# Kernel optimization log

Measured on AMD Instinct MI355X. Metric: run time of the kernel, lower is better.

Reference implementation:

```python
import jax, jax.numpy as jnp
import numpy as np

B, N_FEAT, SEQ, E, H, V = 32, 196, 64, 1024, 1024, 32000


def setup_inputs() -> dict:
    key = jax.random.key(0)
    ks = jax.random.split(key, 16)
    s = 0.02
    return {
        "features": jax.random.normal(ks[0], (B, N_FEAT, E), jnp.float32),
        "captions": jax.random.randint(ks[1], (B, SEQ), 0, V),
        "max_seq_length": SEQ,
        # decoder embedding table (vocab, embed)
        "emb": jax.random.normal(ks[2], (V, E), jnp.float32) * s,
        # attention MLP: Linear(E->H), Tanh, Linear(H->1)
        "Wa1": jax.random.normal(ks[3], (H, E), jnp.float32) * s,
        "ba1": jnp.zeros((H,), jnp.float32),
        "Wa2": jax.random.normal(ks[4], (1, H), jnp.float32) * s,
        "ba2": jnp.zeros((1,), jnp.float32),
        # GRU (1 layer), input = concat(word_emb, context) -> E + H
        "W_ih": jax.random.normal(ks[5], (3 * H, E + H), jnp.float32) * s,
        "W_hh": jax.random.normal(ks[6], (3 * H, H), jnp.float32) * s,
        "b_ih": jnp.zeros((3 * H,), jnp.float32),
        "b_hh": jnp.zeros((3 * H,), jnp.float32),
        # output projection Linear(H -> V)
        "W_fc": jax.random.normal(ks[7], (V, H), jnp.float32) * s,
        "b_fc": jnp.zeros((V,), jnp.float32),
    }


def reference(features, captions, max_seq_length, emb, Wa1, ba1, Wa2, ba2,
              W_ih, W_hh, b_ih, b_hh, W_fc, b_fc):
    # words: (B, S, E)
    words = emb[captions]
    # combined: (B, N_FEAT + S, E)
    combined = jnp.concatenate([features, words], axis=1)
    # attention scores over the combined tokens, softmax along token axis
    scores = jnp.tanh(combined @ Wa1.T + ba1) @ Wa2.T + ba2   # (B, M, 1)
    A = jax.nn.softmax(scores, axis=1)                         # (B, M, 1)
    # context h0 = A^T @ combined -> (B, E); used both as GRU h0 and per-step context
    h0 = jnp.sum(A * combined, axis=1)
    context = h0

    def gru_cell(x, h):
        gi = x @ W_ih.T + b_ih          # (B, 3H)
        gh = h @ W_hh.T + b_hh          # (B, 3H)
        ir, iz, inn = jnp.split(gi, 3, axis=-1)
        hr, hz, hn = jnp.split(gh, 3, axis=-1)
        r = jax.nn.sigmoid(ir + hr)
        z = jax.nn.sigmoid(iz + hz)
        n = jnp.tanh(inn + r * hn)
        return (1.0 - z) * n + z * h

    def step(carry, _):
        input_word, h = carry
        x = jnp.concatenate([emb[input_word], context], axis=-1)  # (B, E+H)
        h_new = gru_cell(x, h)
        out = h_new @ W_fc.T + b_fc                               # (B, V)
        # greedy feedback (eval path / no teacher forcing)
        next_word = jnp.argmax(out, axis=-1)
        return (next_word, h_new), out

    init = (captions[:, 0], h0)
    (_, _), outs = jax.lax.scan(step, init, None, length=max_seq_length - 1)
    outs = jnp.transpose(outs, (1, 0, 2))                         # (B, S-1, V)
    bsz = captions.shape[0]
    vocab = W_fc.shape[0]
    outputs = jnp.concatenate(
        [jnp.zeros((bsz, 1, vocab), outs.dtype), outs], axis=1)   # t=0 stays zero
    return outputs, A
```

## Files before the change

kernel.cpp:

```cpp
#include <hip/hip_runtime.h>
#include <hip/hip_bf16.h>

typedef unsigned long long ull;
typedef unsigned int uint;

#define NB 32
#define NFEAT 196
#define SEQL 64
#define ED 1024
#define HD 1024
#define VOC 32000
#define NCOMB 260
#define NROWS (NB*NCOMB)
#define NTILE 2000

typedef __attribute__((ext_vector_type(8))) short s16x8;
typedef __attribute__((ext_vector_type(4))) float f32x4;
typedef __attribute__((ext_vector_type(4))) uint  u32x4;

union FragU { u32x4 u; s16x8 s; };

#define DOT4(acc, wv, xv) acc = fmaf((wv).x,(xv).x, fmaf((wv).y,(xv).y, fmaf((wv).z,(xv).z, fmaf((wv).w,(xv).w,(acc)))))

__device__ __forceinline__ uint enc_f32(float f) {
    uint u = __float_as_uint(f);
    return (u & 0x80000000u) ? ~u : (u | 0x80000000u);
}
__device__ __forceinline__ ull shflxor64(ull v, int m) {
    uint lo = __shfl_xor((uint)v, m);
    uint hi = __shfl_xor((uint)(v >> 32), m);
    return (((ull)hi) << 32) | (ull)lo;
}

__device__ __forceinline__ void split2(float a, float b, uint& hi, uint& lo) {
    __hip_bfloat162 h2 = __float22bfloat162_rn(make_float2(a, b));
    float2 hf = __bfloat1622float2(h2);
    __hip_bfloat162 l2 = __float22bfloat162_rn(make_float2(a - hf.x, b - hf.y));
    hi = *(uint*)&h2;
    lo = *(uint*)&l2;
}

__global__ void __launch_bounds__(256) k_build(
    const float* __restrict__ features, const int* __restrict__ captions,
    const float* __restrict__ emb, float* __restrict__ combined,
    float* __restrict__ out)
{
    const int bid = blockIdx.x;
    const int t = threadIdx.x;
    if (bid < NROWS) {
        const int b = bid / NCOMB;
        const int i = bid - b*NCOMB;
        const float* src = (i < NFEAT)
            ? (features + ((size_t)(b*NFEAT + i))*ED)
            : (emb + (size_t)captions[b*SEQL + (i - NFEAT)]*ED);
        float4* dst4 = (float4*)(combined + (size_t)bid*ED);
        const float4* s4 = (const float4*)src;
        dst4[t] = s4[t];
    } else {
        const int z = bid - NROWS;
        const int m = z*1024 + t*4;
        if (m < NB*VOC) {
            const int b = m / VOC;
            const int v = m - b*VOC;
            float4 zz = make_float4(0.f,0.f,0.f,0.f);
            *(float4*)(out + (size_t)b*((size_t)SEQL*VOC) + v) = zz;
        }
    }
}

__global__ void __launch_bounds__(256) k_pack_w1(
    const float* __restrict__ Wa1, uint* __restrict__ W1hi, uint* __restrict__ W1lo)
{
    const int eid = blockIdx.x*256 + threadIdx.x;
    const int lane = eid & 63;
    const int ks = (eid >> 6) & 31;
    const int ct = eid >> 11;
    const int c = ct*16 + (lane & 15);
    const int k0 = ks*32 + ((lane >> 4) & 3)*4;
    const float4 wa = *(const float4*)&Wa1[(size_t)c*ED + k0];
    const float4 wb = *(const float4*)&Wa1[(size_t)c*ED + k0 + 16];
    uint hi[4], lo[4];
    split2(wa.x, wa.y, hi[0], lo[0]);
    split2(wa.z, wa.w, hi[1], lo[1]);
    split2(wb.x, wb.y, hi[2], lo[2]);
    split2(wb.z, wb.w, hi[3], lo[3]);
    *(u32x4*)&W1hi[(size_t)eid*4] = (u32x4){hi[0], hi[1], hi[2], hi[3]};
    *(u32x4*)&W1lo[(size_t)eid*4] = (u32x4){lo[0], lo[1], lo[2], lo[3]};
}

__global__ void __launch_bounds__(256) k_pack_wfc(
    const float* __restrict__ W_fc, uint* __restrict__ Whi, uint* __restrict__ Wlo)
{
    const int eid = blockIdx.x*256 + threadIdx.x;
    const int lane = eid & 63;
    const int ks = (eid >> 6) & 31;
    const int tile = eid >> 11;
    const int row = tile*16 + (lane & 15);
    const int k0 = ks*32 + ((lane >> 4) & 3)*4;
    const float4 wa = *(const float4*)&W_fc[(size_t)row*HD + k0];
    const float4 wb = *(const float4*)&W_fc[(size_t)row*HD + k0 + 16];
    uint hi[4], lo[4];
    split2(wa.x, wa.y, hi[0], lo[0]);
    split2(wa.z, wa.w, hi[1], lo[1]);
    split2(wb.x, wb.y, hi[2], lo[2]);
    split2(wb.z, wb.w, hi[3], lo[3]);
    *(u32x4*)&Whi[(size_t)eid*4] = (u32x4){hi[0], hi[1], hi[2], hi[3]};
    *(u32x4*)&Wlo[(size_t)eid*4] = (u32x4){lo[0], lo[1], lo[2], lo[3]};
}

__global__ void __launch_bounds__(256) k_attn_mfma(
    const float* __restrict__ combined, const uint* __restrict__ W1hi,
    const uint* __restrict__ W1lo, const float* __restrict__ ba1,
    const float* __restrict__ Wa2, float* __restrict__ partials)
{
    const int t = threadIdx.x;
    const int w = t >> 6, l = t & 63;
    const int lane16 = l & 15, qk = (l >> 4) & 3;
    const int rt = blockIdx.x*4 + w;
    const int cg = blockIdx.y;

    const float* Arow = combined + (size_t)(rt*16 + lane16)*ED;
    const u32x4* bh_base = (const u32x4*)W1hi + (size_t)(cg*4)*32*64 + l;
    const u32x4* bl_base = (const u32x4*)W1lo + (size_t)(cg*4)*32*64 + l;

    f32x4 acc[4];
#pragma unroll
    for (int i = 0; i < 4; ++i) acc[i] = (f32x4){0.f,0.f,0.f,0.f};

#pragma unroll 2
    for (int ks = 0; ks < 32; ++ks) {
        const int k0 = ks*32 + qk*4;
        const float4 aa = *(const float4*)(Arow + k0);
        const float4 ab = *(const float4*)(Arow + k0 + 16);
        FragU ahi, alo;
        uint h0,l0_,h1,l1_,h2,l2_,h3,l3_;
        split2(aa.x, aa.y, h0, l0_);
        split2(aa.z, aa.w, h1, l1_);
        split2(ab.x, ab.y, h2, l2_);
        split2(ab.z, ab.w, h3, l3_);
        ahi.u = (u32x4){h0, h1, h2, h3};
        alo.u = (u32x4){l0_, l1_, l2_, l3_};
#pragma unroll
        for (int i = 0; i < 4; ++i) {
            FragU bh_, bl_;
            bh_.u = bh_base[((size_t)i*32 + ks)*64];
            bl_.u = bl_base[((size_t)i*32 + ks)*64];
            acc[i] = __builtin_amdgcn_mfma_f32_16x16x32_bf16(ahi.s, bh_.s, acc[i], 0, 0, 0);
            acc[i] = __builtin_amdgcn_mfma_f32_16x16x32_bf16(ahi.s, bl_.s, acc[i], 0, 0, 0);
            acc[i] = __builtin_amdgcn_mfma_f32_16x16x32_bf16(alo.s, bh_.s, acc[i], 0, 0, 0);
        }
    }

    float s[4];
#pragma unroll
    for (int r = 0; r < 4; ++r) {
        float sum = 0.f;
#pragma unroll
        for (int i = 0; i < 4; ++i) {
            const int col = cg*64 + i*16 + lane16;
            sum += tanhf(acc[i][r] + ba1[col]) * Wa2[col];
        }
        s[r] = sum;
    }
#pragma unroll
    for (int m = 1; m <= 8; m <<= 1)
#pragma unroll
        for (int r = 0; r < 4; ++r) s[r] += __shfl_xor(s[r], m);
    if (lane16 == 0) {
#pragma unroll
        for (int r = 0; r < 4; ++r)
            partials[(size_t)(rt*16 + qk*4 + r)*16 + cg] = s[r];
    }
}

__global__ void __launch_bounds__(256) k_attn_finish(
    const float* __restrict__ partials, const float* __restrict__ combined,
    const int* __restrict__ captions,
    float* __restrict__ A_out, float* __restrict__ h0,
    float* __restrict__ ctx, ull* __restrict__ slots0)
{
    const int b = blockIdx.x, t = threadIdx.x;
    __shared__ float sc[NCOMB];
    __shared__ float red[256];

    for (int i = t; i < NCOMB; i += 256) {
        float s = 0.f;
        const float* pr = partials + (size_t)(b*NCOMB + i)*16;
#pragma unroll
        for (int g = 0; g < 16; ++g) s += pr[g];
        sc[i] = s;
    }
    __syncthreads();
    float m = -1e30f;
    for (int i = t; i < NCOMB; i += 256) m = fmaxf(m, sc[i]);
    red[t] = m; __syncthreads();
    for (int s2 = 128; s2 > 0; s2 >>= 1) {
        if (t < s2) red[t] = fmaxf(red[t], red[t+s2]);
        __syncthreads();
    }
    m = red[0]; __syncthreads();
    float ssum = 0.f;
    for (int i = t; i < NCOMB; i += 256) { float e = expf(sc[i] - m); sc[i] = e; ssum += e; }
    red[t] = ssum; __syncthreads();
    for (int s2 = 128; s2 > 0; s2 >>= 1) {
        if (t < s2) red[t] += red[t+s2];
        __syncthreads();
    }
    const float S = red[0]; __syncthreads();
    for (int i = t; i < NCOMB; i += 256) {
        const float a = sc[i] / S;
        sc[i] = a;
        A_out[b*NCOMB + i] = a;
    }
    __syncthreads();
    for (int e = t; e < HD; e += 256) {
        float acc = 0.f;
        const float* cb = combined + (size_t)b*NCOMB*ED + e;
        for (int i = 0; i < NCOMB; ++i) acc = fmaf(sc[i], cb[(size_t)i*ED], acc);
        h0[(size_t)b*HD + e] = acc;
        ctx[(size_t)b*HD + e] = acc;
    }
    if (t == 0) {
        slots0[0*NB + b] = (ull)(~(uint)captions[b*SEQL]);
#pragma unroll
        for (int g = 1; g < 8; ++g) slots0[g*NB + b] = 0ull;
    }
}

__global__ void __launch_bounds__(256) k_gru(
    const float* __restrict__ emb, const float* __restrict__ ctx,
    const float* __restrict__ W_ih, const float* __restrict__ W_hh,
    const float* __restrict__ b_ih, const float* __restrict__ b_hh,
    const float* __restrict__ h_prev, float* __restrict__ h_next,
    const ull* __restrict__ slots_prev, ull* __restrict__ slots_cur,
    uint* __restrict__ Hhi, uint* __restrict__ Hlo)
{
    __shared__ int word_s[NB];
    const int t = threadIdx.x;
    if (t < NB) {
        ull best = 0ull;
#pragma unroll
        for (int g = 0; g < 8; ++g) {
            ull k = slots_prev[g*NB + t];
            best = (k > best) ? k : best;
        }
        word_s[t] = (int)(~(uint)best);
    }
    if (blockIdx.x == 0) slots_cur[t] = 0ull;
    __syncthreads();

    const int j = blockIdx.x;
    const int w = t >> 6, l = t & 63;
    const int b0 = w*8;

    float a[4][8];
#pragma unroll
    for (int g = 0; g < 4; ++g)
#pragma unroll
        for (int i = 0; i < 8; ++i) a[g][i] = 0.f;

    const float* Wr = W_ih + (size_t)j*(ED+HD);
    const float* Wz = W_ih + (size_t)(HD + j)*(ED+HD);
    const float* Wn = W_ih + (size_t)(2*HD + j)*(ED+HD);
#pragma unroll
    for (int q = 0; q < 8; ++q) {
        const int k = q*256 + l*4;
        const float4 wr = *(const float4*)(Wr + k);
        const float4 wz = *(const float4*)(Wz + k);
        const float4 wn = *(const float4*)(Wn + k);
#pragma unroll
        for (int i = 0; i < 8; ++i) {
            const int b = b0 + i;
            const float* xs = (q < 4) ? (emb + (size_t)word_s[b]*ED + k)
                                      : (ctx + (size_t)b*HD + (k - ED));
            const float4 xv = *(const float4*)xs;
            DOT4(a[0][i], wr, xv);
            DOT4(a[1][i], wz, xv);
            DOT4(a[2][i], wn, xv);
        }
    }
    const float* Ur = W_hh + (size_t)j*HD;
    const float* Uz = W_hh + (size_t)(HD + j)*HD;
    const float* Un = W_hh + (size_t)(2*HD + j)*HD;
#pragma unroll
    for (int q = 0; q < 4; ++q) {
        const int k = q*256 + l*4;
        const float4 ur = *(const float4*)(Ur + k);
        const float4 uz = *(const float4*)(Uz + k);
        const float4 un = *(const float4*)(Un + k);
#pragma unroll
        for (int i = 0; i < 8; ++i) {
            const int b = b0 + i;
            const float4 hv = *(const float4*)(h_prev + (size_t)b*HD + k);
            DOT4(a[0][i], ur, hv);
            DOT4(a[1][i], uz, hv);
            DOT4(a[3][i], un, hv);
        }
    }
    int s = (l >> 5) & 1;
    int ib = s*4;
    float tA[4][4];
#pragma unroll
    for (int g = 0; g < 4; ++g)
#pragma unroll
        for (int ii = 0; ii < 4; ++ii) {
            const float send = a[g][(1^s)*4 + ii];
            tA[g][ii] = a[g][s*4 + ii] + __shfl_xor(send, 32);
        }
    s = (l >> 4) & 1; ib += s*2;
    float tB[4][2];
#pragma unroll
    for (int g = 0; g < 4; ++g)
#pragma unroll
        for (int jj = 0; jj < 2; ++jj) {
            const float send = tA[g][(1^s)*2 + jj];
            tB[g][jj] = tA[g][s*2 + jj] + __shfl_xor(send, 16);
        }
    s = (l >> 3) & 1; ib += s;
    float fg[4];
#pragma unroll
    for (int g = 0; g < 4; ++g) {
        const float send = tB[g][1^s];
        fg[g] = tB[g][s] + __shfl_xor(send, 8);
    }
#pragma unroll
    for (int mm = 4; mm >= 1; mm >>= 1)
#pragma unroll
        for (int g = 0; g < 4; ++g) fg[g] += __shfl_xor(fg[g], mm);

    if ((l & 7) == 0) {
        const int b = b0 + ib;
        const float rg = 1.f/(1.f + expf(-(fg[0] + b_ih[j]      + b_hh[j])));
        const float zg = 1.f/(1.f + expf(-(fg[1] + b_ih[HD+j]   + b_hh[HD+j])));
        const float ng = tanhf(fg[2] + b_ih[2*HD+j] + rg*(fg[3] + b_hh[2*HD+j]));
        const float hp = h_prev[(size_t)b*HD + j];
        const float hv = (1.f - zg)*ng + zg*hp;
        h_next[(size_t)b*HD + j] = hv;
        __hip_bfloat16 hb = __float2bfloat16(hv);
        const float hf = __bfloat162float(hb);
        __hip_bfloat16 lb = __float2bfloat16(hv - hf);
        const int bh = b >> 4;
        const int ks = j >> 5;
        const int qk2 = (j >> 2) & 3;
        const int elem = (j & 3) + 4*((j >> 4) & 1);
        const size_t ei = (((size_t)(bh*32 + ks))*64 + qk2*16 + (b & 15))*8 + elem;
        ((ushort*)Hhi)[ei] = *(const ushort*)&hb;
        ((ushort*)Hlo)[ei] = *(const ushort*)&lb;
    }
}

__global__ void __launch_bounds__(256) k_logits(
    const float* __restrict__ W_fc, const uint* __restrict__ Wfchi,
    const uint* __restrict__ Wfclo, const uint* __restrict__ Hhi,
    const uint* __restrict__ Hlo, const float* __restrict__ b_fc,
    float* __restrict__ out, ull* __restrict__ slots_cur, int tstep, int packed)
{
    __shared__ float sm[32][68];
    const int t = threadIdx.x;
    const int w = t >> 6, l = t & 63;
    const int lane16 = l & 15, qk = (l >> 4) & 3;
    const int tile = blockIdx.x*4 + w;
    const int row = tile*16 + lane16;

    const u32x4* hh0 = (const u32x4*)Hhi + l;
    const u32x4* hl0 = (const u32x4*)Hlo + l;
    const u32x4* hh1 = (const u32x4*)Hhi + 2048 + l;
    const u32x4* hl1 = (const u32x4*)Hlo + 2048 + l;

    f32x4 acc0 = {0.f,0.f,0.f,0.f};
    f32x4 acc1 = {0.f,0.f,0.f,0.f};

    if (packed) {
        const u32x4* WH = (const u32x4*)Wfchi + (size_t)tile*32*64 + l;
        const u32x4* WL = (const u32x4*)Wfclo + (size_t)tile*32*64 + l;
#pragma unroll 2
        for (int ks = 0; ks < 32; ++ks) {
            FragU whi, wlo, b0h, b0l, b1h, b1l;
            whi.u = WH[ks*64];
            wlo.u = WL[ks*64];
            b0h.u = hh0[ks*64];
            b0l.u = hl0[ks*64];
            b1h.u = hh1[ks*64];
            b1l.u = hl1[ks*64];
            acc0 = __builtin_amdgcn_mfma_f32_16x16x32_bf16(whi.s, b0h.s, acc0, 0, 0, 0);
            acc0 = __builtin_amdgcn_mfma_f32_16x16x32_bf16(whi.s, b0l.s, acc0, 0, 0, 0);
            acc0 = __builtin_amdgcn_mfma_f32_16x16x32_bf16(wlo.s, b0h.s, acc0, 0, 0, 0);
            acc1 = __builtin_amdgcn_mfma_f32_16x16x32_bf16(whi.s, b1h.s, acc1, 0, 0, 0);
            acc1 = __builtin_amdgcn_mfma_f32_16x16x32_bf16(whi.s, b1l.s, acc1, 0, 0, 0);
            acc1 = __builtin_amdgcn_mfma_f32_16x16x32_bf16(wlo.s, b1h.s, acc1, 0, 0, 0);
        }
    } else {
        const float* Wrow = W_fc + (size_t)row*HD;
#pragma unroll 2
        for (int ks = 0; ks < 32; ++ks) {
            const int k0 = ks*32 + qk*4;
            const float4 wa = *(const float4*)(Wrow + k0);
            const float4 wb = *(const float4*)(Wrow + k0 + 16);
            FragU whi, wlo;
            uint h0,l0_,h1,l1_,h2,l2_,h3,l3_;
            split2(wa.x, wa.y, h0, l0_);
            split2(wa.z, wa.w, h1, l1_);
            split2(wb.x, wb.y, h2, l2_);
            split2(wb.z, wb.w, h3, l3_);
            whi.u = (u32x4){h0, h1, h2, h3};
            wlo.u = (u32x4){l0_, l1_, l2_, l3_};
            FragU b0h, b0l, b1h, b1l;
            b0h.u = hh0[ks*64];
            b0l.u = hl0[ks*64];
            b1h.u = hh1[ks*64];
            b1l.u = hl1[ks*64];
            acc0 = __builtin_amdgcn_mfma_f32_16x16x32_bf16(whi.s, b0h.s, acc0, 0, 0, 0);
            acc0 = __builtin_amdgcn_mfma_f32_16x16x32_bf16(whi.s, b0l.s, acc0, 0, 0, 0);
            acc0 = __builtin_amdgcn_mfma_f32_16x16x32_bf16(wlo.s, b0h.s, acc0, 0, 0, 0);
            acc1 = __builtin_amdgcn_mfma_f32_16x16x32_bf16(whi.s, b1h.s, acc1, 0, 0, 0);
            acc1 = __builtin_amdgcn_mfma_f32_16x16x32_bf16(whi.s, b1l.s, acc1, 0, 0, 0);
            acc1 = __builtin_amdgcn_mfma_f32_16x16x32_bf16(wlo.s, b1h.s, acc1, 0, 0, 0);
        }
    }

    {
        const int rbase = w*16 + qk*4;
        const float4 bias = *(const float4*)&b_fc[blockIdx.x*64 + rbase];
        *(float4*)&sm[lane16][rbase] = make_float4(
            acc0[0] + bias.x, acc0[1] + bias.y, acc0[2] + bias.z, acc0[3] + bias.w);
        *(float4*)&sm[16 + lane16][rbase] = make_float4(
            acc1[0] + bias.x, acc1[1] + bias.y, acc1[2] + bias.z, acc1[3] + bias.w);
    }
    __syncthreads();
    {
        const int b = t >> 3;
        const int rl0 = (t & 7)*8;
        const int vbase = blockIdx.x*64 + rl0;
        float v[8];
        ull bk = 0ull;
#pragma unroll
        for (int e = 0; e < 8; ++e) {
            v[e] = sm[b][rl0 + e];
            const ull key = (((ull)enc_f32(v[e])) << 32) | (ull)(~(uint)(vbase + e));
            bk = (key > bk) ? key : bk;
        }
        float* dst = out + (size_t)b*((size_t)SEQL*VOC) + (size_t)tstep*VOC + vbase;
        ((float4*)dst)[0] = make_float4(v[0], v[1], v[2], v[3]);
        ((float4*)dst)[1] = make_float4(v[4], v[5], v[6], v[7]);
#pragma unroll
        for (int mm = 4; mm >= 1; mm >>= 1) {
            const ull o = shflxor64(bk, mm);
            bk = (o > bk) ? o : bk;
        }
        if ((t & 7) == 0) atomicMax(slots_cur + (blockIdx.x & 7)*NB + b, bk);
    }
}

extern "C" void kernel_launch(void* const* d_in, const int* in_sizes, int n_in,
                              void* d_out, int out_size, void* d_ws, size_t ws_size,
                              hipStream_t stream)
{
    const float* features = (const float*)d_in[0];
    const int*   captions = (const int*)d_in[1];
    const float* emb  = (const float*)d_in[3];
    const float* Wa1  = (const float*)d_in[4];
    const float* ba1  = (const float*)d_in[5];
    const float* Wa2  = (const float*)d_in[6];
    const float* W_ih = (const float*)d_in[8];
    const float* W_hh = (const float*)d_in[9];
    const float* b_ih = (const float*)d_in[10];
    const float* b_hh = (const float*)d_in[11];
    const float* W_fc = (const float*)d_in[12];
    const float* b_fc = (const float*)d_in[13];

    float* out = (float*)d_out;
    float* A_out = out + (size_t)NB*SEQL*VOC;

    char* wsp = (char*)d_ws;
    float* combined = (float*)wsp;  wsp += (size_t)NROWS*ED*4;
    float* partials = (float*)wsp;  wsp += (size_t)NROWS*16*4;
    float* hbuf0    = (float*)wsp;  wsp += (size_t)NB*HD*4;
    float* hbuf1    = (float*)wsp;  wsp += (size_t)NB*HD*4;
    float* ctx      = (float*)wsp;  wsp += (size_t)NB*HD*4;
    ull*   slots    = (ull*)wsp;    wsp += 2*8*NB*sizeof(ull);
    uint*  Hhi      = (uint*)wsp;   wsp += (size_t)4096*16;
    uint*  Hlo      = (uint*)wsp;   wsp += (size_t)4096*16;
    uint*  W1hi     = (uint*)wsp;   wsp += (size_t)131072*16;
    uint*  W1lo     = (uint*)wsp;   wsp += (size_t)131072*16;
    uint*  Wfchi    = (uint*)wsp;   wsp += (size_t)NTILE*32*64*16;
    uint*  Wfclo    = (uint*)wsp;   wsp += (size_t)NTILE*32*64*16;
    size_t packed_need = (size_t)(wsp - (char*)d_ws);
    const int packed = (ws_size >= packed_need) ? 1 : 0;

    k_build<<<NROWS + 1000, 256, 0, stream>>>(features, captions, emb, combined, out);
    k_pack_w1<<<512, 256, 0, stream>>>(Wa1, W1hi, W1lo);
    if (packed)
        k_pack_wfc<<<NTILE*32*64/256, 256, 0, stream>>>(W_fc, Wfchi, Wfclo);
    k_attn_mfma<<<dim3(130, 16), 256, 0, stream>>>(combined, W1hi, W1lo, ba1, Wa2, partials);
    k_attn_finish<<<NB, 256, 0, stream>>>(partials, combined, captions,
                                          A_out, hbuf0, ctx, slots);
    for (int t = 1; t < SEQL; ++t) {
        const float* hp = (t & 1) ? hbuf0 : hbuf1;
        float*       hn = (t & 1) ? hbuf1 : hbuf0;
        const ull* sp = slots + (size_t)((t - 1) & 1)*8*NB;
        ull*       scur = slots + (size_t)(t & 1)*8*NB;
        k_gru<<<1024, 256, 0, stream>>>(emb, ctx, W_ih, W_hh, b_ih, b_hh,
                                        hp, hn, sp, scur, Hhi, Hlo);
        k_logits<<<500, 256, 0, stream>>>(W_fc, Wfchi, Wfclo, Hhi, Hlo, b_fc,
                                          out, scur, t, packed);
    }
}
```

Measured before the change: 4.442 ms.

## Hoist loop-invariant context GRU input projection out of recurrence; widen attention tiles

The context half of the GRU input projection (W_ih[:, E:] @ ctx + b_ih) does not change across timesteps. It is now computed once in a new k_gictx kernel and read back inside each k_gru step. This halves the W_ih bytes streamed per step at the cost of a small 3H×B workspace buffer. The attention MFMA kernel also has each block cover two column groups, which reuses the split A fragments. Output stores now use nontemporal hints.

```diff
diff --git a/kernel.cpp b/kernel.cpp
--- a/kernel.cpp
+++ b/kernel.cpp
@@ -38,6 +38,11 @@
     __hip_bfloat162 l2 = __float22bfloat162_rn(make_float2(a - hf.x, b - hf.y));
     hi = *(uint*)&h2;
     lo = *(uint*)&l2;
+}
+
+__device__ __forceinline__ void nt_store4(float* p, float a, float b, float c, float d) {
+    f32x4 v = {a, b, c, d};
+    __builtin_nontemporal_store(v, (f32x4*)p);
 }
 
 __global__ void __launch_bounds__(256) k_build(
@@ -62,8 +67,7 @@
         if (m < NB*VOC) {
             const int b = m / VOC;
             const int v = m - b*VOC;
-            float4 zz = make_float4(0.f,0.f,0.f,0.f);
-            *(float4*)(out + (size_t)b*((size_t)SEQL*VOC) + v) = zz;
+            nt_store4(out + (size_t)b*((size_t)SEQL*VOC) + v, 0.f, 0.f, 0.f, 0.f);
         }
     }
 }
@@ -117,15 +121,17 @@
     const int w = t >> 6, l = t & 63;
     const int lane16 = l & 15, qk = (l >> 4) & 3;
     const int rt = blockIdx.x*4 + w;
-    const int cg = blockIdx.y;
+    const int cg0 = blockIdx.y*2;
 
     const float* Arow = combined + (size_t)(rt*16 + lane16)*ED;
-    const u32x4* bh_base = (const u32x4*)W1hi + (size_t)(cg*4)*32*64 + l;
-    const u32x4* bl_base = (const u32x4*)W1lo + (size_t)(cg*4)*32*64 + l;
-
-    f32x4 acc[4];
-#pragma unroll
-    for (int i = 0; i < 4; ++i) acc[i] = (f32x4){0.f,0.f,0.f,0.f};
+    const u32x4* bh_base = (const u32x4*)W1hi + l;
+    const u32x4* bl_base = (const u32x4*)W1lo + l;
+
+    f32x4 acc[2][4];
+#pragma unroll
+    for (int c = 0; c < 2; ++c)
+#pragma unroll
+        for (int i = 0; i < 4; ++i) acc[c][i] = (f32x4){0.f,0.f,0.f,0.f};
 
 #pragma unroll 2
     for (int ks = 0; ks < 32; ++ks) {
@@ -141,35 +147,43 @@
         ahi.u = (u32x4){h0, h1, h2, h3};
         alo.u = (u32x4){l0_, l1_, l2_, l3_};
 #pragma unroll
-        for (int i = 0; i < 4; ++i) {
-            FragU bh_, bl_;
-            bh_.u = bh_base[((size_t)i*32 + ks)*64];
-            bl_.u = bl_base[((size_t)i*32 + ks)*64];
-            acc[i] = __builtin_amdgcn_mfma_f32_16x16x32_bf16(ahi.s, bh_.s, acc[i], 0, 0, 0);
-            acc[i] = __builtin_amdgcn_mfma_f32_16x16x32_bf16(ahi.s, bl_.s, acc[i], 0, 0, 0);
-            acc[i] = __builtin_amdgcn_mfma_f32_16x16x32_bf16(alo.s, bh_.s, acc[i], 0, 0, 0);
-        }
-    }
-
-    float s[4];
-#pragma unroll
-    for (int r = 0; r < 4; ++r) {
-        float sum = 0.f;
-#pragma unroll
-        for (int i = 0; i < 4; ++i) {
-            const int col = cg*64 + i*16 + lane16;
-            sum += tanhf(acc[i][r] + ba1[col]) * Wa2[col];
-        }
-        s[r] = sum;
-    }
-#pragma unroll
-    for (int m = 1; m <= 8; m <<= 1)
-#pragma unroll
-        for (int r = 0; r < 4; ++r) s[r] += __shfl_xor(s[r], m);
-    if (lane16 == 0) {
-#pragma unroll
-        for (int r = 0; r < 4; ++r)
-            partials[(size_t)(rt*16 + qk*4 + r)*16 + cg] = s[r];
+        for (int c = 0; c < 2; ++c) {
+#pragma unroll
+            for (int i = 0; i < 4; ++i) {
+                const size_t idx = (((size_t)((cg0 + c)*4 + i))*32 + ks)*64;
+                FragU bh_, bl_;
+                bh_.u = bh_base[idx];
+                bl_.u = bl_base[idx];
+                acc[c][i] = __builtin_amdgcn_mfma_f32_16x16x32_bf16(ahi.s, bh_.s, acc[c][i], 0, 0, 0);
+                acc[c][i] = __builtin_amdgcn_mfma_f32_16x16x32_bf16(ahi.s, bl_.s, acc[c][i], 0, 0, 0);
+                acc[c][i] = __builtin_amdgcn_mfma_f32_16x16x32_bf16(alo.s, bh_.s, acc[c][i], 0, 0, 0);
+            }
+        }
+    }
+
+#pragma unroll
+    for (int c = 0; c < 2; ++c) {
+        const int cg = cg0 + c;
+        float s[4];
+#pragma unroll
+        for (int r = 0; r < 4; ++r) {
+            float sum = 0.f;
+#pragma unroll
+            for (int i = 0; i < 4; ++i) {
+                const int col = cg*64 + i*16 + lane16;
+                sum += tanhf(acc[c][i][r] + ba1[col]) * Wa2[col];
+            }
+            s[r] = sum;
+        }
+#pragma unroll
+        for (int m = 1; m <= 8; m <<= 1)
+#pragma unroll
+            for (int r = 0; r < 4; ++r) s[r] += __shfl_xor(s[r], m);
+        if (lane16 == 0) {
+#pragma unroll
+            for (int r = 0; r < 4; ++r)
+                partials[(size_t)(rt*16 + qk*4 + r)*16 + cg] = s[r];
+        }
     }
 }
 
@@ -227,10 +241,60 @@
     }
 }
 
+__global__ void __launch_bounds__(256) k_gictx(
+    const float* __restrict__ W_ih, const float* __restrict__ b_ih,
+    const float* __restrict__ ctx, float* __restrict__ gictx)
+{
+    const int jj = blockIdx.x;
+    const int t = threadIdx.x;
+    const int w = t >> 6, l = t & 63;
+    const int b0 = w*8;
+    const float* Wrow = W_ih + (size_t)jj*(ED+HD) + ED;
+
+    float a[8];
+#pragma unroll
+    for (int i = 0; i < 8; ++i) a[i] = 0.f;
+#pragma unroll
+    for (int q = 0; q < 4; ++q) {
+        const int k = q*256 + l*4;
+        const float4 wv = *(const float4*)(Wrow + k);
+#pragma unroll
+        for (int i = 0; i < 8; ++i) {
+            const float4 xv = *(const float4*)(ctx + (size_t)(b0 + i)*HD + k);
+            DOT4(a[i], wv, xv);
+        }
+    }
+    int s = (l >> 5) & 1;
+    int ib = s*4;
+    float tA[4];
+#pragma unroll
+    for (int ii = 0; ii < 4; ++ii) {
+        const float send = a[(1^s)*4 + ii];
+        tA[ii] = a[s*4 + ii] + __shfl_xor(send, 32);
+    }
+    s = (l >> 4) & 1; ib += s*2;
+    float tB[2];
+#pragma unroll
+    for (int jj2 = 0; jj2 < 2; ++jj2) {
+        const float send = tA[(1^s)*2 + jj2];
+        tB[jj2] = tA[s*2 + jj2] + __shfl_xor(send, 16);
+    }
+    s = (l >> 3) & 1; ib += s;
+    float fg;
+    {
+        const float send = tB[1^s];
+        fg = tB[s] + __shfl_xor(send, 8);
+    }
+#pragma unroll
+    for (int mm = 4; mm >= 1; mm >>= 1) fg += __shfl_xor(fg, mm);
+    if ((l & 7) == 0)
+        gictx[(size_t)jj*NB + (b0 + ib)] = fg + b_ih[jj];
+}
+
 __global__ void __launch_bounds__(256) k_gru(
-    const float* __restrict__ emb, const float* __restrict__ ctx,
-    const float* __restrict__ W_ih, const float* __restrict__ W_hh,
-    const float* __restrict__ b_ih, const float* __restrict__ b_hh,
+    const float* __restrict__ emb, const float* __restrict__ W_ih,
+    const float* __restrict__ W_hh, const float* __restrict__ gictx,
+    const float* __restrict__ b_hh,
     const float* __restrict__ h_prev, float* __restrict__ h_next,
     const ull* __restrict__ slots_prev, ull* __restrict__ slots_cur,
     uint* __restrict__ Hhi, uint* __restrict__ Hlo)
@@ -263,17 +327,14 @@
     const float* Wz = W_ih + (size_t)(HD + j)*(ED+HD);
     const float* Wn = W_ih + (size_t)(2*HD + j)*(ED+HD);
 #pragma unroll
-    for (int q = 0; q < 8; ++q) {
+    for (int q = 0; q < 4; ++q) {
         const int k = q*256 + l*4;
         const float4 wr = *(const float4*)(Wr + k);
         const float4 wz = *(const float4*)(Wz + k);
         const float4 wn = *(const float4*)(Wn + k);
 #pragma unroll
         for (int i = 0; i < 8; ++i) {
-            const int b = b0 + i;
-            const float* xs = (q < 4) ? (emb + (size_t)word_s[b]*ED + k)
-                                      : (ctx + (size_t)b*HD + (k - ED));
-            const float4 xv = *(const float4*)xs;
+            const float4 xv = *(const float4*)(emb + (size_t)word_s[b0+i]*ED + k);
             DOT4(a[0][i], wr, xv);
             DOT4(a[1][i], wz, xv);
             DOT4(a[2][i], wn, xv);
@@ -290,8 +351,7 @@
         const float4 un = *(const float4*)(Un + k);
 #pragma unroll
         for (int i = 0; i < 8; ++i) {
-            const int b = b0 + i;
-            const float4 hv = *(const float4*)(h_prev + (size_t)b*HD + k);
+            const float4 hv = *(const float4*)(h_prev + (size_t)(b0+i)*HD + k);
             DOT4(a[0][i], ur, hv);
             DOT4(a[1][i], uz, hv);
             DOT4(a[3][i], un, hv);
@@ -330,9 +390,12 @@
 
     if ((l & 7) == 0) {
         const int b = b0 + ib;
-        const float rg = 1.f/(1.f + expf(-(fg[0] + b_ih[j]      + b_hh[j])));
-        const float zg = 1.f/(1.f + expf(-(fg[1] + b_ih[HD+j]   + b_hh[HD+j])));
-        const float ng = tanhf(fg[2] + b_ih[2*HD+j] + rg*(fg[3] + b_hh[2*HD+j]));
+        const float gcr = gictx[(size_t)j*NB + b];
+        const float gcz = gictx[(size_t)(HD + j)*NB + b];
+        const float gcn = gictx[(size_t)(2*HD + j)*NB + b];
+        const float rg = 1.f/(1.f + expf(-(fg[0] + gcr + b_hh[j])));
+        const float zg = 1.f/(1.f + expf(-(fg[1] + gcz + b_hh[HD+j])));
+        const float ng = tanhf(fg[2] + gcn + rg*(fg[3] + b_hh[2*HD+j]));
         const float hp = h_prev[(size_t)b*HD + j];
         const float hv = (1.f - zg)*ng + zg*hp;
         h_next[(size_t)b*HD + j] = hv;
@@ -360,7 +423,6 @@
     const int w = t >> 6, l = t & 63;
     const int lane16 = l & 15, qk = (l >> 4) & 3;
     const int tile = blockIdx.x*4 + w;
-    const int row = tile*16 + lane16;
 
     const u32x4* hh0 = (const u32x4*)Hhi + l;
     const u32x4* hl0 = (const u32x4*)Hlo + l;
@@ -390,7 +452,7 @@
             acc1 = __builtin_amdgcn_mfma_f32_16x16x32_bf16(wlo.s, b1h.s, acc1, 0, 0, 0);
         }
     } else {
-        const float* Wrow = W_fc + (size_t)row*HD;
+        const float* Wrow = W_fc + (size_t)(tile*16 + lane16)*HD;
 #pragma unroll 2
         for (int ks = 0; ks < 32; ++ks) {
             const int k0 = ks*32 + qk*4;
@@ -440,8 +502,8 @@
             bk = (key > bk) ? key : bk;
         }
         float* dst = out + (size_t)b*((size_t)SEQL*VOC) + (size_t)tstep*VOC + vbase;
-        ((float4*)dst)[0] = make_float4(v[0], v[1], v[2], v[3]);
-        ((float4*)dst)[1] = make_float4(v[4], v[5], v[6], v[7]);
+        nt_store4(dst,     v[0], v[1], v[2], v[3]);
+        nt_store4(dst + 4, v[4], v[5], v[6], v[7]);
 #pragma unroll
         for (int mm = 4; mm >= 1; mm >>= 1) {
             const ull o = shflxor64(bk, mm);
@@ -482,6 +544,7 @@
     uint*  Hlo      = (uint*)wsp;   wsp += (size_t)4096*16;
     uint*  W1hi     = (uint*)wsp;   wsp += (size_t)131072*16;
     uint*  W1lo     = (uint*)wsp;   wsp += (size_t)131072*16;
+    float* gictx    = (float*)wsp;  wsp += (size_t)3*HD*NB*4;
     uint*  Wfchi    = (uint*)wsp;   wsp += (size_t)NTILE*32*64*16;
     uint*  Wfclo    = (uint*)wsp;   wsp += (size_t)NTILE*32*64*16;
     size_t packed_need = (size_t)(wsp - (char*)d_ws);
@@ -491,17 +554,18 @@
     k_pack_w1<<<512, 256, 0, stream>>>(Wa1, W1hi, W1lo);
     if (packed)
         k_pack_wfc<<<NTILE*32*64/256, 256, 0, stream>>>(W_fc, Wfchi, Wfclo);
-    k_attn_mfma<<<dim3(130, 16), 256, 0, stream>>>(combined, W1hi, W1lo, ba1, Wa2, partials);
+    k_attn_mfma<<<dim3(130, 8), 256, 0, stream>>>(combined, W1hi, W1lo, ba1, Wa2, partials);
     k_attn_finish<<<NB, 256, 0, stream>>>(partials, combined, captions,
                                           A_out, hbuf0, ctx, slots);
+    k_gictx<<<3*HD, 256, 0, stream>>>(W_ih, b_ih, ctx, gictx);
     for (int t = 1; t < SEQL; ++t) {
         const float* hp = (t & 1) ? hbuf0 : hbuf1;
         float*       hn = (t & 1) ? hbuf1 : hbuf0;
         const ull* sp = slots + (size_t)((t - 1) & 1)*8*NB;
         ull*       scur = slots + (size_t)(t & 1)*8*NB;
-        k_gru<<<1024, 256, 0, stream>>>(emb, ctx, W_ih, W_hh, b_ih, b_hh,
+        k_gru<<<1024, 256, 0, stream>>>(emb, W_ih, W_hh, gictx, b_hh,
                                         hp, hn, sp, scur, Hhi, Hlo);
-        k_logits<<<500, 256, 0, stream>>>(W_fc, Wfchi, Wfclo, Hhi, Hlo, b_fc,
-                                          out, scur, t, packed);
-    }
-}
+        k_logits<<<NTILE/4, 256, 0, stream>>>(W_fc, Wfchi, Wfclo, Hhi, Hlo, b_fc,
+                                              out, scur, t, packed);
+    }
+}
```

Result: faster. 3.844 ms (-13.5%).
